# Kernel optimization log

Hardware: AMD Instinct MI355X
Metric: run time of the kernel (lower is better)

The kernel has to match this reference:

```python
import jax, jax.numpy as jnp
import numpy as np

B, N, M = 4, 4096, 4096


def setup_inputs() -> dict:
    key = jax.random.key(0)
    k1, k2 = jax.random.split(key)
    source = jax.random.normal(k1, (B, N, 3), dtype=jnp.float32)
    target = jax.random.normal(k2, (B, M, 3), dtype=jnp.float32)
    return {"source": source, "target": target}


def reference(source, target):
    # Pairwise squared distances: dist[b, n, m] = ||source[b,n] - target[b,m]||^2
    x2 = jnp.sum(source * source, axis=-1)          # (B, N)
    y2 = jnp.sum(target * target, axis=-1)          # (B, M)
    xy = jnp.einsum('bnd,bmd->bnm', source, target)  # (B, N, M)
    dist = x2[:, :, None] + y2[:, None, :] - 2.0 * xy
    # bidirectional Chamfer (default args: bidirectional=True, reverse=False)
    loss_s2t = jnp.mean(jnp.min(dist, axis=2), axis=1)  # (B,)
    loss_t2s = jnp.mean(jnp.min(dist, axis=1), axis=1)  # (B,)
    return jnp.mean(loss_s2t + loss_t2s)
```

## Files before the change

### kernel.cpp

```cpp
#include <hip/hip_runtime.h>

typedef float f2 __attribute__((ext_vector_type(2)));

namespace {
constexpr int kB = 4;
constexpr int kN = 4096;
constexpr int kPts = kB * kN;
constexpr int kP = 2 * kPts;
constexpr int kBlk = 256;
constexpr int kSplit = 16;
constexpr int kChunk = kN / kSplit;
constexpr float kInf = 3.4e38f;
}


__device__ __forceinline__ unsigned enc(float f) {
  unsigned u = __float_as_uint(f);
  return (u & 0x80000000u) ? ~u : (u | 0x80000000u);
}
__device__ __forceinline__ float dec(unsigned k) {
  return __uint_as_float((k & 0x80000000u) ? (k ^ 0x80000000u) : ~k);
}

__global__ __launch_bounds__(kBlk) void cham_prep_kernel(
    const float* __restrict__ src, const float* __restrict__ tgt,
    float* __restrict__ packf, unsigned* __restrict__ keys,
    float* __restrict__ out) {
  int i = blockIdx.x * kBlk + threadIdx.x;
  const float* p =
      (i < kPts) ? (tgt + (size_t)i * 3) : (src + (size_t)(i - kPts) * 3);
  float x = p[0], y = p[1], z = p[2];
  float w = fmaf(x, x, fmaf(y, y, z * z));
  float* base = packf + (size_t)(i >> 1) * 8 + (i & 1);
  base[0] = x;
  base[2] = y;
  base[4] = z;
  base[6] = w;
  keys[i] = 0xFFFFFFFFu;
  if (i == 0) out[0] = 0.0f;
}

__global__ __launch_bounds__(kBlk) void cham_min_kernel(
    const float* __restrict__ src, const float* __restrict__ tgt,
    const float4* __restrict__ pack4, unsigned* __restrict__ keys) {
  const int dir = blockIdx.z;
  const int b = blockIdx.y;
  const int chunk = blockIdx.x & (kSplit - 1);
  const int ntile = blockIdx.x >> 4;
  const int n = ntile * kBlk + threadIdx.x;

  const float* __restrict__ own = dir ? tgt : src;
  const float* p = own + ((size_t)b * kN + n) * 3;
  const float x = p[0], y = p[1], z = p[2];
  const float w = fmaf(x, x, fmaf(y, y, z * z));
  const f2 NX = {-2.0f * x, -2.0f * x};
  const f2 NY = {-2.0f * y, -2.0f * y};
  const f2 NZ = {-2.0f * z, -2.0f * z};

  const size_t g0 = ((size_t)dir * kPts + (size_t)b * kN + chunk * kChunk) / 2;
  const float4* __restrict__ q = pack4 + 2 * g0;

  float e0 = kInf, e1 = kInf, e2 = kInf, e3 = kInf;
#pragma unroll 8
  for (int g = 0; g < kChunk / 2; ++g) {
    const float4 A = q[2 * g + 0];
    const float4 Bv = q[2 * g + 1];
    const f2 X = {A.x, A.y}, Y = {A.z, A.w};
    const f2 Z = {Bv.x, Bv.y}, W = {Bv.z, Bv.w};
    f2 e = __builtin_elementwise_fma(
               NX, X, __builtin_elementwise_fma(NY, Y, NZ * Z)) +
           W;
    float m = fminf(e.x, e.y);
    switch (g & 3) {
      case 0: e0 = fminf(e0, m); break;
      case 1: e1 = fminf(e1, m); break;
      case 2: e2 = fminf(e2, m); break;
      default: e3 = fminf(e3, m); break;
    }
  }

  const float best = fminf(fminf(e0, e1), fminf(e2, e3)) + w;
  atomicMin(&keys[((size_t)dir * kB + b) * kN + n], enc(best));
}

__global__ __launch_bounds__(kBlk) void cham_reduce_kernel(
    const unsigned* __restrict__ keys, float* __restrict__ out) {
  __shared__ float red[kBlk];
  float acc = 0.0f;
  for (int i = blockIdx.x * kBlk + threadIdx.x; i < kP; i += gridDim.x * kBlk)
    acc += dec(keys[i]);
  red[threadIdx.x] = acc;
  __syncthreads();
  for (int s = kBlk / 2; s > 0; s >>= 1) {
    if (threadIdx.x < s) red[threadIdx.x] += red[threadIdx.x + s];
    __syncthreads();
  }
  if (threadIdx.x == 0) atomicAdd(out, red[0] * (1.0f / kPts));
}

extern "C" void kernel_launch(void* const* d_in, const int* in_sizes, int n_in,
                              void* d_out, int out_size, void* d_ws,
                              size_t ws_size, hipStream_t stream) {
  const float* src = (const float*)d_in[0];
  const float* tgt = (const float*)d_in[1];
  float* out = (float*)d_out;

  unsigned* keys = (unsigned*)d_ws;
  float* packf = (float*)((char*)d_ws + (size_t)kP * 4);

  cham_prep_kernel<<<dim3(kP / kBlk), kBlk, 0, stream>>>(src, tgt, packf, keys,
                                                         out);

  dim3 grid(kN / kBlk * kSplit, kB, 2);
  cham_min_kernel<<<grid, kBlk, 0, stream>>>(src, tgt, (const float4*)packf,
                                             keys);

  cham_reduce_kernel<<<dim3(16), kBlk, 0, stream>>>(keys, out);
}
```

Baseline: 74.29 us.

## Compute two own points per thread to reuse each loaded target pair

Each thread now handles two query points, loaded from the packed buffer, so every streamed float4 pair of candidate points feeds twice as many FMAs. This halves grid size and the number of loads per distance evaluation. The w term is folded into the FMA chain. The prep kernel is also vectorized to process two points per thread with wider loads and stores. The tradeoff is fewer blocks in flight and more registers per thread, which can lower occupancy.

```diff
diff --git a/kernel.cpp b/kernel.cpp
--- a/kernel.cpp
+++ b/kernel.cpp
@@ -10,6 +10,7 @@
 constexpr int kBlk = 256;
 constexpr int kSplit = 16;
 constexpr int kChunk = kN / kSplit;
+constexpr int kOP = 2;
 constexpr float kInf = 3.4e38f;
 }
 
@@ -24,63 +25,76 @@
 
 __global__ __launch_bounds__(kBlk) void cham_prep_kernel(
     const float* __restrict__ src, const float* __restrict__ tgt,
-    float* __restrict__ packf, unsigned* __restrict__ keys,
+    float4* __restrict__ pack4, unsigned* __restrict__ keys,
     float* __restrict__ out) {
-  int i = blockIdx.x * kBlk + threadIdx.x;
-  const float* p =
-      (i < kPts) ? (tgt + (size_t)i * 3) : (src + (size_t)(i - kPts) * 3);
-  float x = p[0], y = p[1], z = p[2];
-  float w = fmaf(x, x, fmaf(y, y, z * z));
-  float* base = packf + (size_t)(i >> 1) * 8 + (i & 1);
-  base[0] = x;
-  base[2] = y;
-  base[4] = z;
-  base[6] = w;
-  keys[i] = 0xFFFFFFFFu;
-  if (i == 0) out[0] = 0.0f;
+  int g = blockIdx.x * kBlk + threadIdx.x;
+  const float* p = (g < kPts / 2) ? (tgt + (size_t)g * 6)
+                                  : (src + (size_t)(g - kPts / 2) * 6);
+  const f2 a = *(const f2*)(p);
+  const f2 bv = *(const f2*)(p + 2);
+  const f2 c = *(const f2*)(p + 4);
+  const float x0 = a.x, y0 = a.y, z0 = bv.x;
+  const float x1 = bv.y, y1 = c.x, z1 = c.y;
+  const float w0 = fmaf(x0, x0, fmaf(y0, y0, z0 * z0));
+  const float w1 = fmaf(x1, x1, fmaf(y1, y1, z1 * z1));
+  pack4[2 * g] = make_float4(x0, x1, y0, y1);
+  pack4[2 * g + 1] = make_float4(z0, z1, w0, w1);
+  ((uint2*)keys)[g] = make_uint2(0xFFFFFFFFu, 0xFFFFFFFFu);
+  if (g == 0) out[0] = 0.0f;
 }
 
 __global__ __launch_bounds__(kBlk) void cham_min_kernel(
-    const float* __restrict__ src, const float* __restrict__ tgt,
     const float4* __restrict__ pack4, unsigned* __restrict__ keys) {
   const int dir = blockIdx.z;
   const int b = blockIdx.y;
   const int chunk = blockIdx.x & (kSplit - 1);
   const int ntile = blockIdx.x >> 4;
-  const int n = ntile * kBlk + threadIdx.x;
+  const int tp = ntile * kBlk + threadIdx.x;
 
-  const float* __restrict__ own = dir ? tgt : src;
-  const float* p = own + ((size_t)b * kN + n) * 3;
-  const float x = p[0], y = p[1], z = p[2];
-  const float w = fmaf(x, x, fmaf(y, y, z * z));
-  const f2 NX = {-2.0f * x, -2.0f * x};
-  const f2 NY = {-2.0f * y, -2.0f * y};
-  const f2 NZ = {-2.0f * z, -2.0f * z};
+  const size_t ownPair =
+      ((size_t)(1 - dir) * kPts + (size_t)b * kN) / 2 + (size_t)tp;
+  const float4 OA = pack4[2 * ownPair];
+  const float4 OB = pack4[2 * ownPair + 1];
+  const f2 NX0 = {-2.0f * OA.x, -2.0f * OA.x};
+  const f2 NY0 = {-2.0f * OA.z, -2.0f * OA.z};
+  const f2 NZ0 = {-2.0f * OB.x, -2.0f * OB.x};
+  const f2 NX1 = {-2.0f * OA.y, -2.0f * OA.y};
+  const f2 NY1 = {-2.0f * OA.w, -2.0f * OA.w};
+  const f2 NZ1 = {-2.0f * OB.y, -2.0f * OB.y};
 
-  const size_t g0 = ((size_t)dir * kPts + (size_t)b * kN + chunk * kChunk) / 2;
+  const size_t g0 =
+      ((size_t)dir * kPts + (size_t)b * kN + (size_t)chunk * kChunk) / 2;
   const float4* __restrict__ q = pack4 + 2 * g0;
 
-  float e0 = kInf, e1 = kInf, e2 = kInf, e3 = kInf;
+  float e0a = kInf, e0b = kInf, e1a = kInf, e1b = kInf;
 #pragma unroll 8
   for (int g = 0; g < kChunk / 2; ++g) {
     const float4 A = q[2 * g + 0];
     const float4 Bv = q[2 * g + 1];
-    const f2 X = {A.x, A.y}, Y = {A.z, A.w};
-    const f2 Z = {Bv.x, Bv.y}, W = {Bv.z, Bv.w};
-    f2 e = __builtin_elementwise_fma(
-               NX, X, __builtin_elementwise_fma(NY, Y, NZ * Z)) +
-           W;
-    float m = fminf(e.x, e.y);
-    switch (g & 3) {
-      case 0: e0 = fminf(e0, m); break;
-      case 1: e1 = fminf(e1, m); break;
-      case 2: e2 = fminf(e2, m); break;
-      default: e3 = fminf(e3, m); break;
+    const f2 X = {A.x, A.y}, Y = {A.z, A.w}, Z = {Bv.x, Bv.y};
+    f2 Wv = {Bv.z, Bv.w};
+    f2 d0 = __builtin_elementwise_fma(
+        NX0, X,
+        __builtin_elementwise_fma(NY0, Y,
+                                  __builtin_elementwise_fma(NZ0, Z, Wv)));
+    f2 d1 = __builtin_elementwise_fma(
+        NX1, X,
+        __builtin_elementwise_fma(NY1, Y,
+                                  __builtin_elementwise_fma(NZ1, Z, Wv)));
+    if (g & 1) {
+      e0b = fminf(fminf(d0.x, d0.y), e0b);
+      e1b = fminf(fminf(d1.x, d1.y), e1b);
+    } else {
+      e0a = fminf(fminf(d0.x, d0.y), e0a);
+      e1a = fminf(fminf(d1.x, d1.y), e1a);
     }
   }
 
-  const float best = fminf(fminf(e0, e1), fminf(e2, e3)) + w;
-  atomicMin(&keys[((size_t)dir * kB + b) * kN + n], enc(best));
+  const float best0 = fminf(e0a, e0b) + OB.z;
+  const float best1 = fminf(e1a, e1b) + OB.w;
+  const unsigned kbase = ((unsigned)(dir * kB + b)) * kN + 2u * (unsigned)tp;
+  atomicMin(&keys[kbase + 0], enc(best0));
+  atomicMin(&keys[kbase + 1], enc(best1));
 }
 
 __global__ __launch_bounds__(kBlk) void cham_reduce_kernel(
@@ -108,12 +122,11 @@
   unsigned* keys = (unsigned*)d_ws;
   float* packf = (float*)((char*)d_ws + (size_t)kP * 4);
 
-  cham_prep_kernel<<<dim3(kP / kBlk), kBlk, 0, stream>>>(src, tgt, packf, keys,
-                                                         out);
+  cham_prep_kernel<<<dim3(kP / 2 / kBlk), kBlk, 0, stream>>>(
+      src, tgt, (float4*)packf, keys, out);
 
-  dim3 grid(kN / kBlk * kSplit, kB, 2);
-  cham_min_kernel<<<grid, kBlk, 0, stream>>>(src, tgt, (const float4*)packf,
-                                             keys);
+  dim3 grid(kN / (kBlk * kOP) * kSplit, kB, 2);
+  cham_min_kernel<<<grid, kBlk, 0, stream>>>((const float4*)packf, keys);
 
   cham_reduce_kernel<<<dim3(16), kBlk, 0, stream>>>(keys, out);
 }
```

Measured after the change: 71.54 us. 3.7% less time.
